# Kernel optimization log

Measured on AMD Instinct MI355X. Metric: run time of the kernel, lower is better.

Reference implementation:

```python
import jax, jax.numpy as jnp
import numpy as np

# Physiological constants (IHCPaulick2024 defaults, learnable=False)
FS = 44100.0                      # sampling rate [Hz]
SCALE = 10.0 ** (-105.0 / 20.0)   # stereocilia displacement scaling
GMET_MAX = 30e-9                  # max MET conductance [S]
X0 = 20e-9                        # displacement bias [m]
S0 = 16e-9                        # fast sensitivity [m]
S1 = 35e-9                        # slow sensitivity [m]
EP = 90e-3                        # endocochlear potential [V]
CM = 12.5e-12                     # membrane capacitance [F]
GKF = 19.8e-9                     # fast K+ conductance [S]
GKS = 19.8e-9                     # slow K+ conductance [S]
EKF = -71e-3                      # fast K+ reversal [V]
EKS = -78e-3                      # slow K+ reversal [V]
V_REST = -57.03e-3                # resting potential [V]
G_PRE = 3.3514e-9                 # pre-charge conductance [S]
PRE_DUR = 0.05                    # pre-charge duration [s]


def setup_inputs() -> dict:
    key = jax.random.key(0)
    # basilar-membrane velocity, shape (B, F, T)
    x = jax.random.normal(key, (8, 50, 131072), dtype=jnp.float32)
    return {"x": x}


def _precharge(dtype):
    """50 ms forward-Euler relaxation with fixed conductance -> steady-state V.
    Identical across (B, F) lanes, so computed as a scalar loop."""
    Ts = 1.0 / FS
    n_pre = int(FS * PRE_DUR)

    def step(_, v):
        Imet = G_PRE * (v - EP)
        Ik = GKF * (v - EKF)
        Is = GKS * (v - EKS)
        return v - (Imet + Ik + Is) * (Ts / CM)

    return jax.lax.fori_loop(0, n_pre, step, jnp.asarray(V_REST, dtype=dtype))


def reference(x):
    Ts = 1.0 / FS
    # 1) stereocilia displacement
    d = SCALE * x                                     # (B, F, T)
    # 2) MET channel conductance: double-exponential sigmoid
    z = X0 - d
    G = GMET_MAX / (1.0 + jnp.exp(z / S1) * (1.0 + jnp.exp(z / S0)))
    # 3) pre-charge to steady state
    v_pre = _precharge(x.dtype)                       # scalar
    V0 = jnp.full(x.shape[:2], v_pre, dtype=x.dtype)  # (B, F)
    # 4) forward-Euler membrane ODE over time (linear recurrence)
    Gt = jnp.moveaxis(G, -1, 0)                       # (T, B, F)

    def step(v, g_t):
        dv = (-g_t * (v - EP) - GKF * (v - EKF) - GKS * (v - EKS)) * (Ts / CM)
        v_new = v + dv
        return v_new, v_new

    _, Vs = jax.lax.scan(step, V0, Gt)                # (T, B, F)
    V = jnp.moveaxis(Vs, 0, -1)                       # (B, F, T)
    return V - v_pre
```

## Files before the change

### kernel.cpp

```cpp
#include <hip/hip_runtime.h>
#include <math.h>

static constexpr double dTS   = 1.0 / 44100.0;
static constexpr double dCM   = 12.5e-12;
static constexpr double dK    = dTS / dCM;
static constexpr double dGKF  = 19.8e-9;
static constexpr double dGKS  = 19.8e-9;
static constexpr double dEKF  = -71e-3;
static constexpr double dEKS  = -78e-3;
static constexpr double dEP   = 90e-3;
static constexpr double dGMET = 30e-9;

static constexpr float F_SCALE = (float)5.623413251903491e-06;
static constexpr float F_X0    = (float)20e-9;
static constexpr float F_INVS1 = (float)(1.0 / 35e-9);
static constexpr float F_INVS0 = (float)(1.0 / 16e-9);
static constexpr float F_ANOG  = (float)(1.0 - (dGKF + dGKS) * dK);
static constexpr float F_GMK   = (float)(dGMET * dK);
static constexpr float F_EP    = (float)dEP;
static constexpr float F_C0    = (float)(dEP + (dGKF * (dEKF - dEP) + dGKS * (dEKS - dEP)) * dK);

constexpr int T_LEN = 131072;
constexpr int CHUNK = 8192;
constexpr int WARM  = 1024;
constexpr int SPAN  = CHUNK + WARM;
constexpr int SPT   = 36;
constexpr int NTH   = 256;

typedef float v4f __attribute__((ext_vector_type(4)));

__device__ __forceinline__ float coef(float xv) {
    float z  = fmaf(-F_SCALE, xv, F_X0);
    float e1 = __expf(z * F_INVS1);
    float e0 = __expf(z * F_INVS0);
    float den = fmaf(e1, e0 + 1.0f, 1.0f);
    float r  = __builtin_amdgcn_rcpf(den);
    return fmaf(-F_GMK, r, F_ANOG);
}

__global__ __launch_bounds__(NTH) void ihc_kernel(const float* __restrict__ x,
                                                  float* __restrict__ out,
                                                  float vpre) {
    const int c = blockIdx.x;
    const int l = blockIdx.y;
    const int t = threadIdx.x;
    const int span_start = c * CHUNK - WARM;
    const long lbase = (long)l * T_LEN;
    const float* xp = x + lbase;
    float* op = out + lbase;
    const int tbase = span_start + t * SPT;

    __shared__ float lbuf[SPAN];
    float4* lb4 = reinterpret_cast<float4*>(lbuf);

#pragma unroll
    for (int j = 0; j < 9; ++j) {
        int g  = t + NTH * j;
        int a0 = span_start + 4 * g;
        int ca = a0 < 0 ? 0 : a0;
        lb4[g] = *reinterpret_cast<const float4*>(xp + ca);
    }
    __syncthreads();

    float4 q[9];
#pragma unroll
    for (int j = 0; j < 9; ++j) q[j] = lb4[t * 9 + j];

    float A = 1.0f, B = 0.0f;
#pragma unroll
    for (int j = 0; j < 9; ++j) {
        float ev[4] = {q[j].x, q[j].y, q[j].z, q[j].w};
#pragma unroll
        for (int i = 0; i < 4; ++i) {
            int g = tbase + 4 * j + i;
            float a = coef(ev[i]);
            a = (g < 0) ? 1.0f : a;
            float b = (g < 0) ? 0.0f : fmaf(-F_EP, a, F_C0);
            B = fmaf(a, B, b);
            A = A * a;
            ev[i] = a;
        }
        q[j] = make_float4(ev[0], ev[1], ev[2], ev[3]);
    }

    const int lane = t & 63;
    const int w    = t >> 6;
#pragma unroll
    for (int d = 1; d < 64; d <<= 1) {
        float pa = __shfl_up(A, d, 64);
        float pb = __shfl_up(B, d, 64);
        if (lane >= d) { B = fmaf(A, pb, B); A = A * pa; }
    }
    __shared__ float wAs[NTH / 64], wBs[NTH / 64];
    if (lane == 63) { wAs[w] = A; wBs[w] = B; }
    __syncthreads();
    float eA = 1.0f, eB = 0.0f;
    for (int i = 0; i < w; ++i) { eB = fmaf(wAs[i], eB, wBs[i]); eA = wAs[i] * eA; }
    float sa = __shfl_up(A, 1, 64);
    float sb = __shfl_up(B, 1, 64);
    if (lane == 0) { sa = 1.0f; sb = 0.0f; }

    float u = fmaf(eA, vpre, eB);
    float v = fmaf(sa, u, sb);

#pragma unroll
    for (int j = 0; j < 9; ++j) {
        float ev[4] = {q[j].x, q[j].y, q[j].z, q[j].w};
        float ov[4];
#pragma unroll
        for (int i = 0; i < 4; ++i) {
            int g = tbase + 4 * j + i;
            float a = ev[i];
            float b = (g < 0) ? 0.0f : fmaf(-F_EP, a, F_C0);
            v = fmaf(a, v, b);
            ov[i] = v - vpre;
        }
        int pos = t * SPT + 4 * j - WARM;
        if (pos >= 0)
            lb4[pos >> 2] = make_float4(ov[0], ov[1], ov[2], ov[3]);
    }
    __syncthreads();

    float* opc = op + c * CHUNK;
#pragma unroll
    for (int j = 0; j < 8; ++j) {
        int g = t + NTH * j;
        float4 o = lb4[g];
        v4f ov = { o.x, o.y, o.z, o.w };
        __builtin_nontemporal_store(ov, reinterpret_cast<v4f*>(opc + 4 * g));
    }
}

static float compute_vpre() {
    const float TsCM = (float)dK;
    float v = -57.03e-3f;
    for (int i = 0; i < 2205; ++i) {
        float Imet = 3.3514e-9f * (v - 0.09f);
        float Ik   = 19.8e-9f   * (v + 0.071f);
        float Is   = 19.8e-9f   * (v + 0.078f);
        v = v - (Imet + Ik + Is) * TsCM;
    }
    return v;
}

extern "C" void kernel_launch(void* const* d_in, const int* in_sizes, int n_in,
                              void* d_out, int out_size, void* d_ws, size_t ws_size,
                              hipStream_t stream) {
    const float* x = (const float*)d_in[0];
    float* out = (float*)d_out;
    const int lanes = in_sizes[0] / T_LEN;
    const int nchunks = T_LEN / CHUNK;
    float vpre = compute_vpre();
    dim3 grid(nchunks, lanes);
    hipLaunchKernelGGL(ihc_kernel, grid, dim3(NTH), 0, stream, x, out, vpre);
}
```

Before: 355.3 us.

## Shrink warm-up to one sample per thread, load inputs directly, swizzle LDS stores

Shrinks the warm-up prefix from 1024 to 256 samples. Each thread now handles a single warm-up sample, whose coefficients are combined through a parallel wave/block scan instead of being processed serially in every thread's span. Inputs are loaded straight from global memory into registers rather than staged through LDS, and the output staging writes use an XOR swizzle to avoid bank conflicts. The sigmoid is also rewritten algebraically as 1+e1+e2 using exp2, and the kernel gets an occupancy hint of 5 blocks per SIMD. The shorter warm-up truncates the decayed initial-state contribution more aggressively, which risks accuracy, and the direct strided per-thread global loads may coalesce less well.

```diff
diff --git a/kernel.cpp b/kernel.cpp
--- a/kernel.cpp
+++ b/kernel.cpp
@@ -1,81 +1,80 @@
 #include <hip/hip_runtime.h>
 #include <math.h>
 
-static constexpr double dTS   = 1.0 / 44100.0;
-static constexpr double dCM   = 12.5e-12;
-static constexpr double dK    = dTS / dCM;
-static constexpr double dGKF  = 19.8e-9;
-static constexpr double dGKS  = 19.8e-9;
-static constexpr double dEKF  = -71e-3;
-static constexpr double dEKS  = -78e-3;
-static constexpr double dEP   = 90e-3;
-static constexpr double dGMET = 30e-9;
+static constexpr double dTS    = 1.0 / 44100.0;
+static constexpr double dCM    = 12.5e-12;
+static constexpr double dK     = dTS / dCM;
+static constexpr double dGKF   = 19.8e-9;
+static constexpr double dGKS   = 19.8e-9;
+static constexpr double dEKF   = -71e-3;
+static constexpr double dEKS   = -78e-3;
+static constexpr double dEP    = 90e-3;
+static constexpr double dGMET  = 30e-9;
+static constexpr double dSCALE = 5.623413251903491e-06;
+static constexpr double dX0    = 20e-9;
+static constexpr double dS0    = 16e-9;
+static constexpr double dS1    = 35e-9;
+static constexpr double dL2E   = 1.4426950408889634;
 
-static constexpr float F_SCALE = (float)5.623413251903491e-06;
-static constexpr float F_X0    = (float)20e-9;
-static constexpr float F_INVS1 = (float)(1.0 / 35e-9);
-static constexpr float F_INVS0 = (float)(1.0 / 16e-9);
-static constexpr float F_ANOG  = (float)(1.0 - (dGKF + dGKS) * dK);
-static constexpr float F_GMK   = (float)(dGMET * dK);
-static constexpr float F_EP    = (float)dEP;
-static constexpr float F_C0    = (float)(dEP + (dGKF * (dEKF - dEP) + dGKS * (dEKS - dEP)) * dK);
+static constexpr float F_K1   = (float)(-dSCALE / dS1 * dL2E);
+static constexpr float F_C1   = (float)( dX0    / dS1 * dL2E);
+static constexpr float F_K2   = (float)(-dSCALE * (1.0/dS1 + 1.0/dS0) * dL2E);
+static constexpr float F_C2   = (float)( dX0    * (1.0/dS1 + 1.0/dS0) * dL2E);
+static constexpr float F_ANOG = (float)(1.0 - (dGKF + dGKS) * dK);
+static constexpr float F_GMK  = (float)(dGMET * dK);
+static constexpr float F_EP   = (float)dEP;
+static constexpr float F_C0   = (float)(dEP + (dGKF*(dEKF-dEP) + dGKS*(dEKS-dEP)) * dK);
 
 constexpr int T_LEN = 131072;
 constexpr int CHUNK = 8192;
-constexpr int WARM  = 1024;
-constexpr int SPAN  = CHUNK + WARM;
-constexpr int SPT   = 36;
+constexpr int WARM  = 256;
+constexpr int SPT   = 32;
 constexpr int NTH   = 256;
 
 typedef float v4f __attribute__((ext_vector_type(4)));
 
 __device__ __forceinline__ float coef(float xv) {
-    float z  = fmaf(-F_SCALE, xv, F_X0);
-    float e1 = __expf(z * F_INVS1);
-    float e0 = __expf(z * F_INVS0);
-    float den = fmaf(e1, e0 + 1.0f, 1.0f);
-    float r  = __builtin_amdgcn_rcpf(den);
-    return fmaf(-F_GMK, r, F_ANOG);
+    float e1  = __builtin_amdgcn_exp2f(fmaf(F_K1, xv, F_C1));
+    float e2  = __builtin_amdgcn_exp2f(fmaf(F_K2, xv, F_C2));
+    float den = 1.0f + e1 + e2;
+    return fmaf(-F_GMK, __builtin_amdgcn_rcpf(den), F_ANOG);
 }
 
-__global__ __launch_bounds__(NTH) void ihc_kernel(const float* __restrict__ x,
-                                                  float* __restrict__ out,
-                                                  float vpre) {
+__global__ __launch_bounds__(NTH, 5) void ihc_kernel(const float* __restrict__ x,
+                                                     float* __restrict__ out,
+                                                     float vpre) {
     const int c = blockIdx.x;
     const int l = blockIdx.y;
     const int t = threadIdx.x;
-    const int span_start = c * CHUNK - WARM;
     const long lbase = (long)l * T_LEN;
-    const float* xp = x + lbase;
-    float* op = out + lbase;
-    const int tbase = span_start + t * SPT;
+    const float* xp  = x + lbase + (long)c * CHUNK;
+    float* opc       = out + lbase + (long)c * CHUNK;
 
-    __shared__ float lbuf[SPAN];
+    __shared__ float lbuf[CHUNK];
     float4* lb4 = reinterpret_cast<float4*>(lbuf);
 
+    float4 q[8];
+    const float4* qp = reinterpret_cast<const float4*>(xp + t * SPT);
 #pragma unroll
-    for (int j = 0; j < 9; ++j) {
-        int g  = t + NTH * j;
-        int a0 = span_start + 4 * g;
-        int ca = a0 < 0 ? 0 : a0;
-        lb4[g] = *reinterpret_cast<const float4*>(xp + ca);
+    for (int j = 0; j < 8; ++j) q[j] = qp[j];
+
+    float aw, bw;
+    {
+        const int woff = (c == 0) ? 0 : -WARM;
+        float wx = xp[t + woff];
+        aw = coef(wx);
+        bw = fmaf(-F_EP, aw, F_C0);
+        if (c == 0) { aw = 1.0f; bw = 0.0f; }
     }
-    __syncthreads();
-
-    float4 q[9];
-#pragma unroll
-    for (int j = 0; j < 9; ++j) q[j] = lb4[t * 9 + j];
 
     float A = 1.0f, B = 0.0f;
 #pragma unroll
-    for (int j = 0; j < 9; ++j) {
+    for (int j = 0; j < 8; ++j) {
         float ev[4] = {q[j].x, q[j].y, q[j].z, q[j].w};
 #pragma unroll
         for (int i = 0; i < 4; ++i) {
-            int g = tbase + 4 * j + i;
             float a = coef(ev[i]);
-            a = (g < 0) ? 1.0f : a;
-            float b = (g < 0) ? 0.0f : fmaf(-F_EP, a, F_C0);
+            float b = fmaf(-F_EP, a, F_C0);
             B = fmaf(a, B, b);
             A = A * a;
             ev[i] = a;
@@ -87,45 +86,57 @@
     const int w    = t >> 6;
 #pragma unroll
     for (int d = 1; d < 64; d <<= 1) {
-        float pa = __shfl_up(A, d, 64);
-        float pb = __shfl_up(B, d, 64);
-        if (lane >= d) { B = fmaf(A, pb, B); A = A * pa; }
+        float pa  = __shfl_up(A,  d, 64);
+        float pb  = __shfl_up(B,  d, 64);
+        float pwa = __shfl_up(aw, d, 64);
+        float pwb = __shfl_up(bw, d, 64);
+        if (lane >= d) {
+            B  = fmaf(A,  pb,  B);  A  *= pa;
+            bw = fmaf(aw, pwb, bw); aw *= pwa;
+        }
     }
-    __shared__ float wAs[NTH / 64], wBs[NTH / 64];
-    if (lane == 63) { wAs[w] = A; wBs[w] = B; }
+
+    if (lane == 63) {
+        lbuf[w]      = aw;  lbuf[4 + w]  = bw;
+        lbuf[8 + w]  = A;   lbuf[12 + w] = B;
+    }
     __syncthreads();
+
+    float wA = 1.0f, wB = 0.0f;
+#pragma unroll
+    for (int i = 0; i < 4; ++i) { wB = fmaf(lbuf[i], wB, lbuf[4 + i]); wA *= lbuf[i]; }
     float eA = 1.0f, eB = 0.0f;
-    for (int i = 0; i < w; ++i) { eB = fmaf(wAs[i], eB, wBs[i]); eA = wAs[i] * eA; }
+    for (int i = 0; i < w; ++i) { eB = fmaf(lbuf[8 + i], eB, lbuf[12 + i]); eA *= lbuf[8 + i]; }
     float sa = __shfl_up(A, 1, 64);
     float sb = __shfl_up(B, 1, 64);
     if (lane == 0) { sa = 1.0f; sb = 0.0f; }
 
-    float u = fmaf(eA, vpre, eB);
-    float v = fmaf(sa, u, sb);
+    float vw = fmaf(wA, vpre, wB);
+    float u  = fmaf(eA, vw, eB);
+    float v  = fmaf(sa, u, sb);
+    __syncthreads();
 
+    const int s = t & 7;
 #pragma unroll
-    for (int j = 0; j < 9; ++j) {
+    for (int j = 0; j < 8; ++j) {
         float ev[4] = {q[j].x, q[j].y, q[j].z, q[j].w};
         float ov[4];
 #pragma unroll
         for (int i = 0; i < 4; ++i) {
-            int g = tbase + 4 * j + i;
             float a = ev[i];
-            float b = (g < 0) ? 0.0f : fmaf(-F_EP, a, F_C0);
+            float b = fmaf(-F_EP, a, F_C0);
             v = fmaf(a, v, b);
             ov[i] = v - vpre;
         }
-        int pos = t * SPT + 4 * j - WARM;
-        if (pos >= 0)
-            lb4[pos >> 2] = make_float4(ov[0], ov[1], ov[2], ov[3]);
+        lb4[t * 8 + (j ^ s)] = make_float4(ov[0], ov[1], ov[2], ov[3]);
     }
     __syncthreads();
 
-    float* opc = op + c * CHUNK;
 #pragma unroll
     for (int j = 0; j < 8; ++j) {
-        int g = t + NTH * j;
-        float4 o = lb4[g];
+        int g  = t + NTH * j;
+        int gp = g ^ ((g >> 3) & 7);
+        float4 o = lb4[gp];
         v4f ov = { o.x, o.y, o.z, o.w };
         __builtin_nontemporal_store(ov, reinterpret_cast<v4f*>(opc + 4 * g));
     }
```

Result: faster. 346.5 us (-2.5%).
